# Kernel optimization log

Measured on AMD Instinct MI355X. Metric: run time of the kernel, lower is better.

## Reference

```python
import jax, jax.numpy as jnp
import numpy as np

B, SQ, SK, H, HEADS, E, DFF = 4, 512, 1024, 1024, 16, 8, 4096
DH = H // HEADS
EPS = 1e-6


def _ln(x, g, b):
    m = jnp.mean(x, -1, keepdims=True)
    v = jnp.mean((x - m) ** 2, -1, keepdims=True)
    return (x - m) * jax.lax.rsqrt(v + EPS) * g + b


def setup_inputs() -> dict:
    key = jax.random.key(0)
    ks = jax.random.split(key, 16)
    s = 0.02
    return {
        "concated_input": jax.random.normal(ks[0], (B, SK, H), jnp.float32),
        "gen_emb": jax.random.normal(ks[1], (B, SQ, H), jnp.float32),
        "mask": jnp.zeros((B, 1, SQ, SK), jnp.float32),
        "ln_g": jnp.ones((H,), jnp.float32),
        "ln_b": jnp.zeros((H,), jnp.float32),
        "wq": jax.random.normal(ks[2], (H, H), jnp.float32) * s,
        "bq": jnp.zeros((H,), jnp.float32),
        "wk": jax.random.normal(ks[3], (H, H), jnp.float32) * s,
        "bk": jnp.zeros((H,), jnp.float32),
        "wv": jax.random.normal(ks[4], (H, H), jnp.float32) * s,
        "bv": jnp.zeros((H,), jnp.float32),
        "wo": jax.random.normal(ks[5], (H, H), jnp.float32) * s,
        "bo": jnp.zeros((H,), jnp.float32),
        "gw": jax.random.normal(ks[6], (H, E), jnp.float32) * s,
        "gb": jnp.zeros((E,), jnp.float32),
        "w1": jax.random.normal(ks[7], (E, H, DFF), jnp.float32) * s,
        "b1": jnp.zeros((E, DFF), jnp.float32),
        "w2": jax.random.normal(ks[8], (E, DFF, H), jnp.float32) * s,
        "b2": jnp.zeros((E, H), jnp.float32),
    }


def reference(concated_input, gen_emb, mask, ln_g, ln_b, wq, bq, wk, bk, wv, bv,
              wo, bo, gw, gb, w1, b1, w2, b2):
    residual_gen = gen_emb
    ctx_ln = _ln(concated_input, ln_g, ln_b)
    gen_ln = _ln(gen_emb, ln_g, ln_b)

    # multi-head cross attention: gen queries, concated keys/values
    q = (gen_ln @ wq + bq).reshape(B, SQ, HEADS, DH).transpose(0, 2, 1, 3)
    k = (ctx_ln @ wk + bk).reshape(B, SK, HEADS, DH).transpose(0, 2, 1, 3)
    v = (ctx_ln @ wv + bv).reshape(B, SK, HEADS, DH).transpose(0, 2, 1, 3)
    scores = jnp.einsum("bhqd,bhkd->bhqk", q, k) / np.sqrt(DH).astype(np.float32)
    attn = jax.nn.softmax(scores + mask, axis=-1)
    ctx_v = jnp.einsum("bhqk,bhkd->bhqd", attn, v)
    ctx_v = ctx_v.transpose(0, 2, 1, 3).reshape(B, SQ, H)
    ca_out = ctx_v @ wo + bo + residual_gen

    ln_ca = _ln(ca_out, ln_g, ln_b)

    # top-1 router on ca_out (pre-LN, as in original)
    gate = jax.nn.softmax(ca_out @ gw + gb, axis=-1)
    top_idx = jnp.argmax(gate, axis=-1)  # [B,SQ]

    # dense all-expert FFN, then gather selected expert (faithful to original)
    h1 = jax.nn.gelu(jnp.einsum("bsh,ehf->bsef", ln_ca, w1) + b1, approximate=False)
    expert_out = jnp.einsum("bsef,efh->bseh", h1, w2) + b2  # [B,SQ,E,H]
    sel = jnp.take_along_axis(expert_out, top_idx[:, :, None, None], axis=2)
    moe_out = sel[:, :, 0, :] + ln_ca
    return moe_out
```

## Files before the change

kernel.cpp:

```cpp
#include <hip/hip_runtime.h>
#include <stdint.h>
#include <stddef.h>

typedef _Float16 f16;
typedef _Float16 half8 __attribute__((ext_vector_type(8)));
typedef float f32x4 __attribute__((ext_vector_type(4)));

constexpr int kB = 4, kSQ = 512, kSK = 1024, kH = 1024, kHeads = 16, kE = 8, kDFF = 4096;
constexpr int kTok = kB * kSQ;

__device__ __forceinline__ void g2l16(const f16* g, f16* l) {
  __builtin_amdgcn_global_load_lds((const __attribute__((address_space(1))) uint32_t*)g,
                                   (__attribute__((address_space(3))) uint32_t*)l, 16, 0, 0);
}

__device__ __forceinline__ int xcd_swz(int phys, int nwg) {
  return (phys & 7) * (nwg >> 3) + (phys >> 3);
}

struct TrAllP {
  const float* w1; const float* w2;
  const float* wq; const float* wk; const float* wv; const float* wo;
  f16* w1_t; f16* w2_t; f16* wq_t; f16* wk_t; f16* wv_t; f16* wo_t;
};
__global__ __launch_bounds__(256) void tr_all(TrAllP tp) {
  __shared__ float t[2][64 * 65];
  int z = blockIdx.z;
  int ft = blockIdx.x;
  const float* src; f16* dst; int R, C, cx4, ry;
  if (z < 8) {
    src = tp.w1 + (long)z * kH * kDFF; dst = tp.w1_t + (long)z * kH * kDFF;
    R = kH; C = kDFF; cx4 = ft & 15; ry = ft >> 4;
  } else if (z < 16) {
    src = tp.w2 + (long)(z - 8) * kDFF * kH; dst = tp.w2_t + (long)(z - 8) * kDFF * kH;
    R = kDFF; C = kH; cx4 = ft & 3; ry = ft >> 2;
  } else {
    int mat = ft >> 6, t2 = ft & 63;
    src = mat == 0 ? tp.wq : mat == 1 ? tp.wk : mat == 2 ? tp.wv : tp.wo;
    dst = mat == 0 ? tp.wq_t : mat == 1 ? tp.wk_t : mat == 2 ? tp.wv_t : tp.wo_t;
    R = kH; C = kH; cx4 = t2 & 3; ry = t2 >> 2;
  }
  int r0 = ry * 64;
  int tid = threadIdx.x;
#pragma unroll
  for (int ct = 0; ct < 4; ct++) {
    int c0 = cx4 * 256 + ct * 64;
    float* tb = t[ct & 1];
#pragma unroll
    for (int s = 0; s < 4; s++) {
      int idx = s * 256 + tid;
      int lr = idx >> 4, lc = (idx & 15) << 2;
      float4 v = *(const float4*)(src + (long)(r0 + lr) * C + c0 + lc);
      tb[lr * 65 + lc] = v.x; tb[lr * 65 + lc + 1] = v.y;
      tb[lr * 65 + lc + 2] = v.z; tb[lr * 65 + lc + 3] = v.w;
    }
    __syncthreads();
#pragma unroll
    for (int s = 0; s < 2; s++) {
      int idx = s * 256 + tid;
      int dr = idx >> 3, dc = (idx & 7) << 3;
      union { f16 h[8]; uint4 u; } o;
#pragma unroll
      for (int j = 0; j < 8; j++) o.h[j] = (f16)tb[(dc + j) * 65 + dr];
      *(uint4*)(dst + (long)(c0 + dr) * R + r0 + dc) = o.u;
    }
  }
}

__global__ __launch_bounds__(256) void ln2_kernel(const float* __restrict__ x0,
                                                  const float* __restrict__ x1,
                                                  const float* __restrict__ g,
                                                  const float* __restrict__ b,
                                                  f16* __restrict__ o0,
                                                  f16* __restrict__ o1, int rows0) {
  int row = blockIdx.x;
  const float* xr;
  f16* orow;
  if (row < rows0) { xr = x0 + (long)row * kH; orow = o0 + (long)row * kH; }
  else { int r2 = row - rows0; xr = x1 + (long)r2 * kH; orow = o1 + (long)r2 * kH; }
  int tid = threadIdx.x;
  float4 v = *(const float4*)(xr + tid * 4);
  float s = v.x + v.y + v.z + v.w;
  float s2 = v.x * v.x + v.y * v.y + v.z * v.z + v.w * v.w;
  __shared__ float red[8];
  for (int o = 32; o; o >>= 1) { s += __shfl_down(s, o); s2 += __shfl_down(s2, o); }
  int wv = tid >> 6, lane = tid & 63;
  if (lane == 0) { red[wv] = s; red[4 + wv] = s2; }
  __syncthreads();
  if (tid == 0) {
    red[0] = red[0] + red[1] + red[2] + red[3];
    red[4] = red[4] + red[5] + red[6] + red[7];
  }
  __syncthreads();
  float mean = red[0] * (1.0f / kH);
  float var = red[4] * (1.0f / kH) - mean * mean;
  float rs = rsqrtf(var + 1e-6f);
  float4 gv = *(const float4*)(g + tid * 4);
  float4 bv = *(const float4*)(b + tid * 4);
  union { f16 h[4]; uint2 u; } o;
  o.h[0] = (f16)((v.x - mean) * rs * gv.x + bv.x);
  o.h[1] = (f16)((v.y - mean) * rs * gv.y + bv.y);
  o.h[2] = (f16)((v.z - mean) * rs * gv.z + bv.z);
  o.h[3] = (f16)((v.w - mean) * rs * gv.w + bv.w);
  *(uint2*)(orow + tid * 4) = o.u;
}

__global__ __launch_bounds__(256) void ln_kernel(const float* __restrict__ x,
                                                 const float* __restrict__ g,
                                                 const float* __restrict__ b,
                                                 f16* __restrict__ oh, float* __restrict__ of,
                                                 int* __restrict__ zc) {
  int row = blockIdx.x;
  int tid = threadIdx.x;
  if (zc && row == 0 && tid < kE) zc[tid] = 0;
  const float* xr = x + (long)row * kH;
  float4 v = *(const float4*)(xr + tid * 4);
  float s = v.x + v.y + v.z + v.w;
  float s2 = v.x * v.x + v.y * v.y + v.z * v.z + v.w * v.w;
  __shared__ float red[8];
  for (int o = 32; o; o >>= 1) { s += __shfl_down(s, o); s2 += __shfl_down(s2, o); }
  int wv = tid >> 6, lane = tid & 63;
  if (lane == 0) { red[wv] = s; red[4 + wv] = s2; }
  __syncthreads();
  if (tid == 0) {
    red[0] = red[0] + red[1] + red[2] + red[3];
    red[4] = red[4] + red[5] + red[6] + red[7];
  }
  __syncthreads();
  float mean = red[0] * (1.0f / kH);
  float var = red[4] * (1.0f / kH) - mean * mean;
  float rs = rsqrtf(var + 1e-6f);
  float4 gv = *(const float4*)(g + tid * 4);
  float4 bv = *(const float4*)(b + tid * 4);
  float y0 = (v.x - mean) * rs * gv.x + bv.x;
  float y1 = (v.y - mean) * rs * gv.y + bv.y;
  float y2 = (v.z - mean) * rs * gv.z + bv.z;
  float y3 = (v.w - mean) * rs * gv.w + bv.w;
  long base = (long)row * kH + tid * 4;
  union { f16 h[4]; uint2 u; } o;
  o.h[0] = (f16)y0; o.h[1] = (f16)y1; o.h[2] = (f16)y2; o.h[3] = (f16)y3;
  *(uint2*)(oh + base) = o.u;
  float4 o4 = {y0, y1, y2, y3};
  *(float4*)(of + base) = o4;
}

__global__ __launch_bounds__(64) void router_kernel(const float* __restrict__ ca,
                                                    const float* __restrict__ gw,
                                                    const float* __restrict__ gb,
                                                    int* __restrict__ cursors,
                                                    int* __restrict__ list,
                                                    int* __restrict__ eid) {
  int t = blockIdx.x;
  int lane = threadIdx.x;
  const float* x = ca + (long)t * kH;
  float acc[kE];
#pragma unroll
  for (int e = 0; e < kE; e++) acc[e] = 0.0f;
  for (int h = lane; h < kH; h += 64) {
    float xv = x[h];
    const float* gr = gw + (long)h * kE;
#pragma unroll
    for (int e = 0; e < kE; e++) acc[e] += xv * gr[e];
  }
#pragma unroll
  for (int e = 0; e < kE; e++)
    for (int o = 32; o; o >>= 1) acc[e] += __shfl_down(acc[e], o);
  if (lane == 0) {
    int best = 0;
    float bv = acc[0] + gb[0];
    for (int e = 1; e < kE; e++) {
      float v = acc[e] + gb[e];
      if (v > bv) { bv = v; best = e; }
    }
    int slot = atomicAdd(&cursors[best], 1);
    list[best * kTok + slot] = t;
    eid[t] = best;
  }
}

__global__ __launch_bounds__(256) void ffn2_reduce(const float* __restrict__ part,
                                                   const float* __restrict__ lnca,
                                                   const float* __restrict__ b2,
                                                   const int* __restrict__ eid,
                                                   float* __restrict__ out) {
  int t = blockIdx.x;
  int i = threadIdx.x * 4;
  int e = eid[t];
  long idx = (long)t * kH + i;
  float4 p0 = *(const float4*)(part + idx);
  float4 p1 = *(const float4*)(part + (long)kTok * kH + idx);
  float4 p2 = *(const float4*)(part + 2L * kTok * kH + idx);
  float4 p3 = *(const float4*)(part + 3L * kTok * kH + idx);
  float4 r  = *(const float4*)(lnca + idx);
  float4 bb = *(const float4*)(b2 + (long)e * kH + i);
  float4 o = {p0.x + p1.x + p2.x + p3.x + r.x + bb.x,
              p0.y + p1.y + p2.y + p3.y + r.y + bb.y,
              p0.z + p1.z + p2.z + p3.z + r.z + bb.z,
              p0.w + p1.w + p2.w + p3.w + r.w + bb.w};
  *(float4*)(out + idx) = o;
}

__global__ __launch_bounds__(256) void flash_kernel(const f16* __restrict__ q,
                                                    const f16* __restrict__ k,
                                                    const f16* __restrict__ v_t,
                                                    const float* __restrict__ mask,
                                                    f16* __restrict__ ctx) {
  __shared__ f16 Ks0[64 * 64], Ks1[64 * 64];
  __shared__ f16 Vs0[64 * 64], Vs1[64 * 64];
  __shared__ f16 Ps[4][16][72];
  int l = xcd_swz(blockIdx.x, gridDim.x);
  int qt = l & 7;
  int bh = l >> 3;
  int b = bh >> 4;
  int ho = (bh & 15) * 64;
  int tid = threadIdx.x, lane = tid & 63, wave = tid >> 6;
  int quad = lane >> 4, lo = lane & 15;

  long qg = ((long)b * kSQ + qt * 64 + wave * 16 + lo) * kH + ho;
  half8 aq0 = *(const half8*)(q + qg + quad * 8);
  half8 aq1 = *(const half8*)(q + qg + 32 + quad * 8);

  int srow = tid >> 3;
  int soct = (tid & 7) ^ (srow & 7);
  const f16* ksrc[2];
  const f16* vsrc[2];
#pragma unroll
  for (int s = 0; s < 2; s++) {
    int r = s * 32 + srow;
    ksrc[s] = k + ((long)b * kSK + r) * kH + ho + soct * 8;
    vsrc[s] = v_t + ((long)bh * 64 + r) * kSK + soct * 8;
  }
  const float* maskp = mask + ((long)b * kSQ + qt * 64 + wave * 16 + quad * 4) * kSK;

  float m_s[4] = {-1e30f, -1e30f, -1e30f, -1e30f};
  float l_s[4] = {0.f, 0.f, 0.f, 0.f};
  f32x4 O[4] = {};

  auto stageKV = [&](f16* Kd, f16* Vd, int sk0) {
#pragma unroll
    for (int s = 0; s < 2; s++) g2l16(ksrc[s] + (long)sk0 * kH, &Kd[(s * 256 + tid) * 8]);
#pragma unroll
    for (int s = 0; s < 2; s++) g2l16(vsrc[s] + sk0, &Vd[(s * 256 + tid) * 8]);
  };
  auto computeT = [&](const f16* Kc, const f16* Vc, int kt) {
    int sk0 = kt * 64;
    f32x4 sf[4] = {};
#pragma unroll
    for (int nt = 0; nt < 4; nt++) {
      int key = nt * 16 + lo;
      half8 bk0 = *(const half8*)&Kc[key * 64 + (((0 * 4 + quad)) ^ (key & 7)) * 8];
      half8 bk1 = *(const half8*)&Kc[key * 64 + (((1 * 4 + quad)) ^ (key & 7)) * 8];
      sf[nt] = __builtin_amdgcn_mfma_f32_16x16x32_f16(aq0, bk0, sf[nt], 0, 0, 0);
      sf[nt] = __builtin_amdgcn_mfma_f32_16x16x32_f16(aq1, bk1, sf[nt], 0, 0, 0);
    }
#pragma unroll
    for (int r = 0; r < 4; r++)
#pragma unroll
      for (int nt = 0; nt < 4; nt++)
        sf[nt][r] += maskp[(long)r * kSK + sk0 + nt * 16 + lo];
#pragma unroll
    for (int r = 0; r < 4; r++) {
      float mx = fmaxf(fmaxf(sf[0][r], sf[1][r]), fmaxf(sf[2][r], sf[3][r]));
      mx = fmaxf(mx, __shfl_xor(mx, 1));
      mx = fmaxf(mx, __shfl_xor(mx, 2));
      mx = fmaxf(mx, __shfl_xor(mx, 4));
      mx = fmaxf(mx, __shfl_xor(mx, 8));
      float m_new = fmaxf(m_s[r], mx);
      float alpha = __expf(m_s[r] - m_new);
      m_s[r] = m_new;
      float p0 = __expf(sf[0][r] - m_new), p1 = __expf(sf[1][r] - m_new);
      float p2 = __expf(sf[2][r] - m_new), p3 = __expf(sf[3][r] - m_new);
      float rs = p0 + p1 + p2 + p3;
      rs += __shfl_xor(rs, 1);
      rs += __shfl_xor(rs, 2);
      rs += __shfl_xor(rs, 4);
      rs += __shfl_xor(rs, 8);
      l_s[r] = l_s[r] * alpha + rs;
#pragma unroll
      for (int nt = 0; nt < 4; nt++) O[nt][r] *= alpha;
      Ps[wave][quad * 4 + r][0 * 16 + lo] = (f16)p0;
      Ps[wave][quad * 4 + r][1 * 16 + lo] = (f16)p1;
      Ps[wave][quad * 4 + r][2 * 16 + lo] = (f16)p2;
      Ps[wave][quad * 4 + r][3 * 16 + lo] = (f16)p3;
    }
    half8 ap0 = *(const half8*)&Ps[wave][lo][quad * 8];
    half8 ap1 = *(const half8*)&Ps[wave][lo][32 + quad * 8];
#pragma unroll
    for (int nt = 0; nt < 4; nt++) {
      int d = nt * 16 + lo;
      half8 bv0 = *(const half8*)&Vc[d * 64 + (((0 * 4 + quad)) ^ (d & 7)) * 8];
      half8 bv1 = *(const half8*)&Vc[d * 64 + (((1 * 4 + quad)) ^ (d & 7)) * 8];
      O[nt] = __builtin_amdgcn_mfma_f32_16x16x32_f16(ap0, bv0, O[nt], 0, 0, 0);
      O[nt] = __builtin_amdgcn_mfma_f32_16x16x32_f16(ap1, bv1, O[nt], 0, 0, 0);
    }
  };

  constexpr int NT = kSK / 64;
  stageKV(Ks0, Vs0, 0);
  __syncthreads();
  for (int kt = 0; kt < NT; kt += 2) {
    if (kt + 1 < NT) stageKV(Ks1, Vs1, (kt + 1) * 64);
    computeT(Ks0, Vs0, kt);
    __syncthreads();
    if (kt + 1 < NT) {
      if (kt + 2 < NT) stageKV(Ks0, Vs0, (kt + 2) * 64);
      computeT(Ks1, Vs1, kt + 1);
      __syncthreads();
    }
  }
#pragma unroll
  for (int r = 0; r < 4; r++) {
    float inv = 1.0f / l_s[r];
    long row = (long)b * kSQ + qt * 64 + wave * 16 + quad * 4 + r;
#pragma unroll
    for (int nt = 0; nt < 4; nt++)
      ctx[row * kH + ho + nt * 16 + lo] = (f16)(O[nt][r] * inv);
  }
}

struct GemmP {
  const f16* A; long a_row, a_z1, a_z2;
  const f16* Bm; long b_nstr, b_z1, b_z2;
  float* Cf; f16* Ch; long c_row, c_z1, c_z2, c_split; int c_tr;
  const float* bias; long bias_z;
  const float* res; long res_row, res_z1, res_z2;
  float alpha; int gelu; int ksplit;
  int M, N, K, zdiv;
  int gx, gy;
  const int* glist; const int* cnt;
};

template <int BM, int BN>
__device__ __forceinline__ void gemm_body(const GemmP& p, int bx, int by, int bz,
                                          f16* A0, f16* A1, f16* B0, f16* B1) {
  constexpr int FM = BM / 32, FN = BN / 64;
  constexpr int SA = BM / 64, SB = BN / 64;
  int z = bz;
  int kb = 0, kEnd = p.K, ks = 0;
  if (p.ksplit > 1) {
    int kc = p.K / p.ksplit;
    ks = z % p.ksplit;
    kb = ks * kc;
    kEnd = kb + kc;
    z /= p.ksplit;
  }
  long aoff = 0, boff = 0, coff = 0, roff = 0, biasoff = 0;
  const int* gl = nullptr;
  int Meff = p.M;
  if (p.glist) {
    Meff = p.cnt[z];
    gl = p.glist + (long)z * kTok;
    boff = (long)z * p.b_z2;
    biasoff = (long)z * p.bias_z;
  } else {
    int z1 = z / p.zdiv, z2 = z % p.zdiv;
    aoff = (long)z1 * p.a_z1 + (long)z2 * p.a_z2;
    boff = (long)z1 * p.b_z1 + (long)z2 * p.b_z2;
    coff = (long)z1 * p.c_z1 + (long)z2 * p.c_z2;
    roff = (long)z1 * p.res_z1 + (long)z2 * p.res_z2;
  }
  coff += (long)ks * p.c_split;
  int m0 = by * BM;
  if (m0 >= Meff) return;
  int n0 = bx * BN;
  int tid = threadIdx.x, lane = tid & 63, wave = tid >> 6;
  int wm = (wave & 1) * (BM / 2), wn = (wave >> 1) * (BN / 4);
  int q = lane >> 4, lo = lane & 15;

  int srow = tid >> 3;
  int soct = (tid & 7) ^ (srow & 7);
  const f16* asrc[SA];
  const f16* bsrc[SB];
#pragma unroll
  for (int s = 0; s < SA; s++) {
    int row = m0 + s * 64 + srow;
    if (gl) row = gl[row < Meff ? row : Meff - 1];
    asrc[s] = p.A + aoff + (long)row * p.a_row + soct * 8;
  }
#pragma unroll
  for (int s = 0; s < SB; s++)
    bsrc[s] = p.Bm + boff + (long)(n0 + s * 64 + srow) * p.b_nstr + soct * 8;

  f32x4 acc[FM][FN] = {};

  auto stage = [&](f16* Ad, f16* Bd, int k0) {
#pragma unroll
    for (int s = 0; s < SA; s++) g2l16(asrc[s] + k0, &Ad[(s * 512 + tid) * 8]);
#pragma unroll
    for (int s = 0; s < SB; s++) g2l16(bsrc[s] + k0, &Bd[(s * 512 + tid) * 8]);
  };
  auto compute = [&](const f16* As, const f16* Bs) {
    half8 af[2][FM], bf[2][FN];
#pragma unroll
    for (int kk = 0; kk < 2; kk++) {
#pragma unroll
      for (int i = 0; i < FM; i++) {
        int r = wm + i * 16 + lo;
        af[kk][i] = *(const half8*)&As[r * 64 + ((kk * 4 + q) ^ (r & 7)) * 8];
      }
#pragma unroll
      for (int j = 0; j < FN; j++) {
        int n = wn + j * 16 + lo;
        bf[kk][j] = *(const half8*)&Bs[n * 64 + ((kk * 4 + q) ^ (n & 7)) * 8];
      }
    }
#pragma unroll
    for (int kk = 0; kk < 2; kk++)
#pragma unroll
      for (int i = 0; i < FM; i++)
#pragma unroll
        for (int j = 0; j < FN; j++)
          acc[i][j] = __builtin_amdgcn_mfma_f32_16x16x32_f16(af[kk][i], bf[kk][j], acc[i][j], 0, 0, 0);
  };

  stage(A0, B0, kb);
  __syncthreads();
  for (int k0 = kb; k0 < kEnd; k0 += 128) {
    if (k0 + 64 < kEnd) stage(A1, B1, k0 + 64);
    compute(A0, B0);
    __syncthreads();
    if (k0 + 64 < kEnd) {
      if (k0 + 128 < kEnd) stage(A0, B0, k0 + 128);
      compute(A1, B1);
      __syncthreads();
    }
  }

#pragma unroll
  for (int i = 0; i < FM; i++) {
#pragma unroll
    for (int j = 0; j < FN; j++) {
      int col = n0 + wn + j * 16 + lo;
      if (p.c_tr) {
        int row0 = m0 + wm + i * 16 + q * 4;
        union { f16 h[4]; uint2 u; } o;
#pragma unroll
        for (int r = 0; r < 4; r++) {
          float v = acc[i][j][r];
          if (p.bias) v += p.bias[biasoff + col];
          v *= p.alpha;
          o.h[r] = (f16)v;
        }
        *(uint2*)&p.Ch[coff + (long)col * p.c_row + row0] = o.u;
      } else {
#pragma unroll
        for (int r = 0; r < 4; r++) {
          int row = m0 + wm + i * 16 + q * 4 + r;
          if (row < Meff) {
            long rr = gl ? (long)gl[row] : (long)row;
            float v = acc[i][j][r];
            if (p.bias) v += p.bias[biasoff + col];
            v *= p.alpha;
            if (p.res) v += p.res[roff + rr * p.res_row + col];
            if (p.gelu) v = 0.5f * v * (1.0f + erff(v * 0.70710678118654752f));
            long ci = coff + rr * p.c_row + col;
            if (p.Cf) p.Cf[ci] = v;
            else p.Ch[ci] = (f16)v;
          }
        }
      }
    }
  }
}

template <int BM, int BN>
__global__ __launch_bounds__(512) void gemm_t(GemmP p) {
  __shared__ f16 A0[BM * 64], A1[BM * 64], B0[BN * 64], B1[BN * 64];
  int l = xcd_swz(blockIdx.x, gridDim.x);
  int bx = l % p.gx;
  int r = l / p.gx;
  int by = r % p.gy;
  int bz = r / p.gy;
  gemm_body<BM, BN>(p, bx, by, bz, A0, A1, B0, B1);
}

struct Multi3P {
  GemmP g0, g1, g2;
  int n0, n1;
  int gx0, gy0, gx1, gy1, gx2, gy2;
};

__global__ __launch_bounds__(512) void gemm_qkv(Multi3P mp) {
  __shared__ f16 A0[128 * 64], A1[128 * 64], B0[128 * 64], B1[128 * 64];
  int fb = xcd_swz(blockIdx.x, gridDim.x);
  if (fb < mp.n0) {
    gemm_body<128, 128>(mp.g0, fb % mp.gx0, (fb / mp.gx0) % mp.gy0, fb / (mp.gx0 * mp.gy0),
                        A0, A1, B0, B1);
    return;
  }
  fb -= mp.n0;
  if (fb < mp.n1) {
    gemm_body<128, 128>(mp.g1, fb % mp.gx1, (fb / mp.gx1) % mp.gy1, fb / (mp.gx1 * mp.gy1),
                        A0, A1, B0, B1);
    return;
  }
  fb -= mp.n1;
  gemm_body<128, 128>(mp.g2, fb % mp.gx2, (fb / mp.gx2) % mp.gy2, fb / (mp.gx2 * mp.gy2),
                      A0, A1, B0, B1);
}

extern "C" void kernel_launch(void* const* d_in, const int* in_sizes, int n_in,
                              void* d_out, int out_size, void* d_ws, size_t ws_size,
                              hipStream_t stream) {
  const float* concated = (const float*)d_in[0];
  const float* gen      = (const float*)d_in[1];
  const float* mask     = (const float*)d_in[2];
  const float* ln_g     = (const float*)d_in[3];
  const float* ln_b     = (const float*)d_in[4];
  const float* wq = (const float*)d_in[5];  const float* bq = (const float*)d_in[6];
  const float* wk = (const float*)d_in[7];  const float* bk = (const float*)d_in[8];
  const float* wv = (const float*)d_in[9];  const float* bv = (const float*)d_in[10];
  const float* wo = (const float*)d_in[11]; const float* bo = (const float*)d_in[12];
  const float* gw = (const float*)d_in[13]; const float* gb = (const float*)d_in[14];
  const float* w1 = (const float*)d_in[15]; const float* b1 = (const float*)d_in[16];
  const float* w2 = (const float*)d_in[17]; const float* b2 = (const float*)d_in[18];
  float* out = (float*)d_out;

  size_t off = 0;
  auto alloc = [&](size_t bytes) -> void* {
    void* p = (char*)d_ws + off;
    off += (bytes + 255) & ~(size_t)255;
    return p;
  };
  f16* wq_t  = (f16*)alloc((size_t)kH * kH * 2);
  f16* wk_t  = (f16*)alloc((size_t)kH * kH * 2);
  f16* wv_t  = (f16*)alloc((size_t)kH * kH * 2);
  f16* wo_t  = (f16*)alloc((size_t)kH * kH * 2);
  f16* w1_t  = (f16*)alloc((size_t)kE * kH * kDFF * 2);
  f16* w2_t  = (f16*)alloc((size_t)kE * kDFF * kH * 2);
  f16* lnc_h = (f16*)alloc((size_t)kB * kSK * kH * 2);
  f16* lng_h = (f16*)alloc((size_t)kTok * kH * 2);
  f16* q_h   = (f16*)alloc((size_t)kTok * kH * 2);
  f16* k_h   = (f16*)alloc((size_t)kB * kSK * kH * 2);
  f16* v_t   = (f16*)alloc((size_t)kB * kSK * kH * 2);
  f16* ctx_h = (f16*)alloc((size_t)kTok * kH * 2);
  float* ca_f   = (float*)alloc((size_t)kTok * kH * 4);
  float* lnca_f = (float*)alloc((size_t)kTok * kH * 4);
  f16* lnca_h   = (f16*)alloc((size_t)kTok * kH * 2);
  f16* h1_h     = (f16*)alloc((size_t)kTok * kDFF * 2);
  float* part_f = (float*)alloc((size_t)4 * kTok * kH * 4);
  int* cnt_d    = (int*)alloc(kE * 4);
  int* list_d   = (int*)alloc((size_t)kE * kTok * 4);
  int* eid_d    = (int*)alloc((size_t)kTok * 4);

  {
    TrAllP tp{w1, w2, wq, wk, wv, wo, w1_t, w2_t, wq_t, wk_t, wv_t, wo_t};
    tr_all<<<dim3(256, 1, 17), 256, 0, stream>>>(tp);
  }

  ln2_kernel<<<kB * kSK + kTok, 256, 0, stream>>>(concated, gen, ln_g, ln_b,
                                                  lnc_h, lng_h, kB * kSK);

  {
    Multi3P mp{};
    GemmP& pq = mp.g0;
    pq.A = lng_h; pq.a_row = kH; pq.Bm = wq_t; pq.b_nstr = kH;
    pq.Ch = q_h; pq.c_row = kH; pq.bias = bq; pq.alpha = 0.125f;
    pq.M = kTok; pq.N = kH; pq.K = kH; pq.zdiv = 1;
    GemmP& pk = mp.g1;
    pk.A = lnc_h; pk.a_row = kH; pk.Bm = wk_t; pk.b_nstr = kH;
    pk.Ch = k_h; pk.c_row = kH; pk.bias = bk; pk.alpha = 1.0f;
    pk.M = kB * kSK; pk.N = kH; pk.K = kH; pk.zdiv = 1;
    GemmP& pv = mp.g2;
    pv.A = lnc_h; pv.a_row = kH; pv.a_z1 = (long)kSK * kH;
    pv.Bm = wv_t; pv.b_nstr = kH;
    pv.Ch = v_t; pv.c_row = kSK; pv.c_z1 = (long)kH * kSK; pv.c_tr = 1;
    pv.bias = bv; pv.alpha = 1.0f;
    pv.M = kSK; pv.N = kH; pv.K = kH; pv.zdiv = 1;
    mp.gx0 = kH / 128; mp.gy0 = kTok / 128;        mp.n0 = mp.gx0 * mp.gy0;
    mp.gx1 = kH / 128; mp.gy1 = (kB * kSK) / 128;  mp.n1 = mp.gx1 * mp.gy1;
    mp.gx2 = kH / 128; mp.gy2 = kSK / 128;
    int ntot = mp.n0 + mp.n1 + mp.gx2 * mp.gy2 * kB;
    gemm_qkv<<<dim3(ntot), 512, 0, stream>>>(mp);
  }
  flash_kernel<<<dim3((kSQ / 64) * kB * kHeads), 256, 0, stream>>>(q_h, k_h, v_t, mask, ctx_h);
  {
    GemmP p{}; p.A = ctx_h; p.a_row = kH;
    p.Bm = wo_t; p.b_nstr = kH;
    p.Cf = ca_f; p.c_row = kH; p.bias = bo;
    p.res = gen; p.res_row = kH;
    p.alpha = 1.0f; p.M = kTok; p.N = kH; p.K = kH; p.zdiv = 1;
    p.gx = kH / 64; p.gy = kTok / 64;
    gemm_t<64, 64><<<dim3(p.gx * p.gy), 512, 0, stream>>>(p);
  }
  ln_kernel<<<kTok, 256, 0, stream>>>(ca_f, ln_g, ln_b, lnca_h, lnca_f, cnt_d);
  router_kernel<<<kTok, 64, 0, stream>>>(ca_f, gw, gb, cnt_d, list_d, eid_d);
  {
    GemmP p{}; p.A = lnca_h; p.a_row = kH;
    p.Bm = w1_t; p.b_nstr = kH; p.b_z2 = (long)kH * kDFF;
    p.Ch = h1_h; p.c_row = kDFF; p.bias = b1; p.bias_z = kDFF;
    p.alpha = 1.0f; p.gelu = 1; p.M = kTok; p.N = kDFF; p.K = kH; p.zdiv = 1;
    p.glist = list_d; p.cnt = cnt_d;
    p.gx = kDFF / 128; p.gy = kTok / 128;
    gemm_t<128, 128><<<dim3(p.gx * p.gy * kE), 512, 0, stream>>>(p);
  }
  {
    GemmP p{}; p.A = h1_h; p.a_row = kDFF;
    p.Bm = w2_t; p.b_nstr = kDFF; p.b_z2 = (long)kDFF * kH;
    p.Cf = part_f; p.c_row = kH; p.c_split = (long)kTok * kH;
    p.alpha = 1.0f; p.ksplit = 4;
    p.M = kTok; p.N = kH; p.K = kDFF; p.zdiv = 1;
    p.glist = list_d; p.cnt = cnt_d;
    p.gx = kH / 128; p.gy = kTok / 128;
    gemm_t<128, 128><<<dim3(p.gx * p.gy * kE * 4), 512, 0, stream>>>(p);
  }
  ffn2_reduce<<<kTok, 256, 0, stream>>>(part_f, lnca_f, b2, eid_d, out);
}
```

Before: 621.7 us.

## Fuse expert weight transposes into QKV GEMM launch to overlap with compute

The large w1/w2 expert weight fp32-to-fp16 transposes move out of the upfront transpose kernel and into extra workgroups of the QKV projection GEMM launch, so this memory-bound work can overlap with the compute-bound GEMM tiles. Only the four small attention matrices are still transposed up front, in a slimmer kernel. The fused kernel shares one LDS buffer between the GEMM and transpose paths. The risk is that transpose blocks compete with GEMM blocks for bandwidth and CU slots, and are scheduled after the GEMM tiles.

After: 745.7 us. 1.2x slower.

```diff
diff --git a/kernel.cpp b/kernel.cpp
--- a/kernel.cpp
+++ b/kernel.cpp
@@ -18,52 +18,34 @@
   return (phys & 7) * (nwg >> 3) + (phys >> 3);
 }
 
-struct TrAllP {
-  const float* w1; const float* w2;
-  const float* wq; const float* wk; const float* wv; const float* wo;
-  f16* w1_t; f16* w2_t; f16* wq_t; f16* wk_t; f16* wv_t; f16* wo_t;
-};
-__global__ __launch_bounds__(256) void tr_all(TrAllP tp) {
-  __shared__ float t[2][64 * 65];
-  int z = blockIdx.z;
+struct Tr4P { const float* s0; const float* s1; const float* s2; const float* s3;
+              f16* d0; f16* d1; f16* d2; f16* d3; };
+__global__ __launch_bounds__(256) void tr4(Tr4P tp) {
+  __shared__ float t[64 * 65];
   int ft = blockIdx.x;
-  const float* src; f16* dst; int R, C, cx4, ry;
-  if (z < 8) {
-    src = tp.w1 + (long)z * kH * kDFF; dst = tp.w1_t + (long)z * kH * kDFF;
-    R = kH; C = kDFF; cx4 = ft & 15; ry = ft >> 4;
-  } else if (z < 16) {
-    src = tp.w2 + (long)(z - 8) * kDFF * kH; dst = tp.w2_t + (long)(z - 8) * kDFF * kH;
-    R = kDFF; C = kH; cx4 = ft & 3; ry = ft >> 2;
-  } else {
-    int mat = ft >> 6, t2 = ft & 63;
-    src = mat == 0 ? tp.wq : mat == 1 ? tp.wk : mat == 2 ? tp.wv : tp.wo;
-    dst = mat == 0 ? tp.wq_t : mat == 1 ? tp.wk_t : mat == 2 ? tp.wv_t : tp.wo_t;
-    R = kH; C = kH; cx4 = t2 & 3; ry = t2 >> 2;
-  }
-  int r0 = ry * 64;
+  int mat = ft >> 8, t2 = ft & 255;
+  const float* src = mat == 0 ? tp.s0 : mat == 1 ? tp.s1 : mat == 2 ? tp.s2 : tp.s3;
+  f16* dst = mat == 0 ? tp.d0 : mat == 1 ? tp.d1 : mat == 2 ? tp.d2 : tp.d3;
+  int cx = t2 & 15, ry = t2 >> 4;
+  int r0 = ry * 64, c0 = cx * 64;
   int tid = threadIdx.x;
 #pragma unroll
-  for (int ct = 0; ct < 4; ct++) {
-    int c0 = cx4 * 256 + ct * 64;
-    float* tb = t[ct & 1];
-#pragma unroll
-    for (int s = 0; s < 4; s++) {
-      int idx = s * 256 + tid;
-      int lr = idx >> 4, lc = (idx & 15) << 2;
-      float4 v = *(const float4*)(src + (long)(r0 + lr) * C + c0 + lc);
-      tb[lr * 65 + lc] = v.x; tb[lr * 65 + lc + 1] = v.y;
-      tb[lr * 65 + lc + 2] = v.z; tb[lr * 65 + lc + 3] = v.w;
-    }
-    __syncthreads();
-#pragma unroll
-    for (int s = 0; s < 2; s++) {
-      int idx = s * 256 + tid;
-      int dr = idx >> 3, dc = (idx & 7) << 3;
-      union { f16 h[8]; uint4 u; } o;
-#pragma unroll
-      for (int j = 0; j < 8; j++) o.h[j] = (f16)tb[(dc + j) * 65 + dr];
-      *(uint4*)(dst + (long)(c0 + dr) * R + r0 + dc) = o.u;
-    }
+  for (int s = 0; s < 4; s++) {
+    int idx = s * 256 + tid;
+    int lr = idx >> 4, lc = (idx & 15) << 2;
+    float4 v = *(const float4*)(src + (long)(r0 + lr) * kH + c0 + lc);
+    t[lr * 65 + lc] = v.x; t[lr * 65 + lc + 1] = v.y;
+    t[lr * 65 + lc + 2] = v.z; t[lr * 65 + lc + 3] = v.w;
+  }
+  __syncthreads();
+#pragma unroll
+  for (int s = 0; s < 2; s++) {
+    int idx = s * 256 + tid;
+    int dr = idx >> 3, dc = (idx & 7) << 3;
+    union { f16 h[8]; uint4 u; } o;
+#pragma unroll
+    for (int j = 0; j < 8; j++) o.h[j] = (f16)t[(dc + j) * 65 + dr];
+    *(uint4*)(dst + (long)(c0 + dr) * kH + r0 + dc) = o.u;
   }
 }
 
@@ -479,24 +461,74 @@
   int n0, n1;
   int gx0, gy0, gx1, gy1, gx2, gy2;
 };
-
-__global__ __launch_bounds__(512) void gemm_qkv(Multi3P mp) {
-  __shared__ f16 A0[128 * 64], A1[128 * 64], B0[128 * 64], B1[128 * 64];
+struct QkvTrP {
+  Multi3P mp;
+  const float* w1; const float* w2;
+  f16* w1_t; f16* w2_t;
+  int nqkv;
+};
+
+__global__ __launch_bounds__(512) void gemm_qkv_tr(QkvTrP P) {
+  __shared__ f16 smem[4 * 128 * 64];
   int fb = xcd_swz(blockIdx.x, gridDim.x);
-  if (fb < mp.n0) {
-    gemm_body<128, 128>(mp.g0, fb % mp.gx0, (fb / mp.gx0) % mp.gy0, fb / (mp.gx0 * mp.gy0),
+  if (fb < P.nqkv) {
+    f16* A0 = smem;
+    f16* A1 = smem + 128 * 64;
+    f16* B0 = smem + 2 * 128 * 64;
+    f16* B1 = smem + 3 * 128 * 64;
+    const Multi3P& mp = P.mp;
+    if (fb < mp.n0) {
+      gemm_body<128, 128>(mp.g0, fb % mp.gx0, (fb / mp.gx0) % mp.gy0, fb / (mp.gx0 * mp.gy0),
+                          A0, A1, B0, B1);
+      return;
+    }
+    fb -= mp.n0;
+    if (fb < mp.n1) {
+      gemm_body<128, 128>(mp.g1, fb % mp.gx1, (fb / mp.gx1) % mp.gy1, fb / (mp.gx1 * mp.gy1),
+                          A0, A1, B0, B1);
+      return;
+    }
+    fb -= mp.n1;
+    gemm_body<128, 128>(mp.g2, fb % mp.gx2, (fb / mp.gx2) % mp.gy2, fb / (mp.gx2 * mp.gy2),
                         A0, A1, B0, B1);
     return;
   }
-  fb -= mp.n0;
-  if (fb < mp.n1) {
-    gemm_body<128, 128>(mp.g1, fb % mp.gx1, (fb / mp.gx1) % mp.gy1, fb / (mp.gx1 * mp.gy1),
-                        A0, A1, B0, B1);
-    return;
-  }
-  fb -= mp.n1;
-  gemm_body<128, 128>(mp.g2, fb % mp.gx2, (fb / mp.gx2) % mp.gy2, fb / (mp.gx2 * mp.gy2),
-                      A0, A1, B0, B1);
+  int tb = fb - P.nqkv;
+  float* t = (float*)smem;
+  const float* src; f16* dst; int R, C, cx4, ry;
+  if (tb < 2048) {
+    int e = tb >> 8, r = tb & 255;
+    src = P.w1 + (long)e * kH * kDFF; dst = P.w1_t + (long)e * kH * kDFF;
+    R = kH; C = kDFF; cx4 = r & 15; ry = r >> 4;
+  } else {
+    int tb2 = tb - 2048;
+    int e = tb2 >> 8, r = tb2 & 255;
+    src = P.w2 + (long)e * kDFF * kH; dst = P.w2_t + (long)e * kDFF * kH;
+    R = kDFF; C = kH; cx4 = r & 3; ry = r >> 2;
+  }
+  int r0 = ry * 64;
+  int tid = threadIdx.x;
+#pragma unroll
+  for (int ct = 0; ct < 4; ct++) {
+    int c0 = cx4 * 256 + ct * 64;
+    float* tb_ = t + (ct & 1) * (64 * 65);
+#pragma unroll
+    for (int s = 0; s < 2; s++) {
+      int idx = s * 512 + tid;
+      int lr = idx >> 4, lc = (idx & 15) << 2;
+      float4 v = *(const float4*)(src + (long)(r0 + lr) * C + c0 + lc);
+      tb_[lr * 65 + lc] = v.x; tb_[lr * 65 + lc + 1] = v.y;
+      tb_[lr * 65 + lc + 2] = v.z; tb_[lr * 65 + lc + 3] = v.w;
+    }
+    __syncthreads();
+    {
+      int dr = tid >> 3, dc = (tid & 7) << 3;
+      union { f16 h[8]; uint4 u; } o;
+#pragma unroll
+      for (int j = 0; j < 8; j++) o.h[j] = (f16)tb_[(dc + j) * 65 + dr];
+      *(uint4*)(dst + (long)(c0 + dr) * R + r0 + dc) = o.u;
+    }
+  }
 }
 
 extern "C" void kernel_launch(void* const* d_in, const int* in_sizes, int n_in,
@@ -544,15 +576,16 @@
   int* eid_d    = (int*)alloc((size_t)kTok * 4);
 
   {
-    TrAllP tp{w1, w2, wq, wk, wv, wo, w1_t, w2_t, wq_t, wk_t, wv_t, wo_t};
-    tr_all<<<dim3(256, 1, 17), 256, 0, stream>>>(tp);
+    Tr4P tp{wq, wk, wv, wo, wq_t, wk_t, wv_t, wo_t};
+    tr4<<<dim3(1024), 256, 0, stream>>>(tp);
   }
 
   ln2_kernel<<<kB * kSK + kTok, 256, 0, stream>>>(concated, gen, ln_g, ln_b,
                                                   lnc_h, lng_h, kB * kSK);
 
   {
-    Multi3P mp{};
+    QkvTrP P{};
+    Multi3P& mp = P.mp;
     GemmP& pq = mp.g0;
     pq.A = lng_h; pq.a_row = kH; pq.Bm = wq_t; pq.b_nstr = kH;
     pq.Ch = q_h; pq.c_row = kH; pq.bias = bq; pq.alpha = 0.125f;
@@ -570,8 +603,10 @@
     mp.gx0 = kH / 128; mp.gy0 = kTok / 128;        mp.n0 = mp.gx0 * mp.gy0;
     mp.gx1 = kH / 128; mp.gy1 = (kB * kSK) / 128;  mp.n1 = mp.gx1 * mp.gy1;
     mp.gx2 = kH / 128; mp.gy2 = kSK / 128;
-    int ntot = mp.n0 + mp.n1 + mp.gx2 * mp.gy2 * kB;
-    gemm_qkv<<<dim3(ntot), 512, 0, stream>>>(mp);
+    P.nqkv = mp.n0 + mp.n1 + mp.gx2 * mp.gy2 * kB;
+    P.w1 = w1; P.w2 = w2; P.w1_t = w1_t; P.w2_t = w2_t;
+    int ntot = P.nqkv + 4096;
+    gemm_qkv_tr<<<dim3(ntot), 512, 0, stream>>>(P);
   }
   flash_kernel<<<dim3((kSQ / 64) * kB * kHeads), 256, 0, stream>>>(q_h, k_h, v_t, mask, ctx_h);
   {
```
